# Optimization experiments

Hardware: AMD Instinct MI355X
Metric: run time of the kernel (lower is better)

Reference implementation:

```python
import jax, jax.numpy as jnp
import numpy as np

N, E = 50000, 800000
IN, HID, OUT, EH = 128, 64, 128, 32  # node dims, edge-MLP hidden=32
N_ETYPES, N_NTYPES = 3, 2


def setup_inputs() -> dict:
    key = jax.random.key(0)
    ks = jax.random.split(key, 12)
    w = lambda k, shape, fan: jax.random.normal(k, shape, jnp.float32) / np.float32(np.sqrt(fan))
    nf = jax.random.normal(ks[0], (N, IN), jnp.float32)
    edge_index = jax.random.randint(ks[1], (2, E), 0, N, dtype=jnp.int32)
    edge_type = jax.random.randint(ks[2], (E,), 0, N_ETYPES, dtype=jnp.int32)
    node_type = jax.random.randint(ks[3], (N,), 0, N_NTYPES, dtype=jnp.int32)
    return {
        "nf": nf,
        "edge_index": edge_index,
        "edge_type": edge_type,
        "node_type": node_type,
        # layer 0: 128 -> 64
        "eW0": w(ks[4], (N_ETYPES, 2 * IN, EH), 2 * IN),
        "eb0": jax.random.normal(ks[5], (N_ETYPES, EH), jnp.float32) * 0.01,
        "nW0": w(ks[6], (N_NTYPES, N_ETYPES * EH, HID), N_ETYPES * EH),
        "nb0": jax.random.normal(ks[7], (N_NTYPES, HID), jnp.float32) * 0.01,
        # layer 1: 64 -> 128
        "eW1": w(ks[8], (N_ETYPES, 2 * HID, EH), 2 * HID),
        "eb1": jax.random.normal(ks[9], (N_ETYPES, EH), jnp.float32) * 0.01,
        "nW1": w(ks[10], (N_NTYPES, N_ETYPES * EH, OUT), N_ETYPES * EH),
        "nb1": jax.random.normal(ks[11], (N_NTYPES, OUT), jnp.float32) * 0.01,
    }


def _layer(nf, eW, eb, nW, nb, src, dst, edge_type, node_type):
    """One GraphNeuralNetLayer: per-edge-type message MLP + mean-scatter, then per-node-type update MLP."""
    n = nf.shape[0]
    # edge gather + concat: [E, 2*in]
    feat = jnp.concatenate([nf[src], nf[dst]], axis=-1)
    msgs = []
    for e in range(eW.shape[0]):  # fixed, small number of edge types
        m = jax.nn.relu(feat @ eW[e] + eb[e])            # [E, EH]
        mask = (edge_type == e).astype(nf.dtype)          # select this edge type
        s = jax.ops.segment_sum(m * mask[:, None], dst, num_segments=n)
        cnt = jax.ops.segment_sum(mask, dst, num_segments=n)
        # mean over mailbox; nodes with no type-e in-edges get zeros
        msgs.append(s / jnp.maximum(cnt, 1.0)[:, None])
    h = jnp.concatenate(msgs, axis=-1)                    # [N, 3*EH]
    out0 = jax.nn.relu(h @ nW[0] + nb[0])
    out1 = jax.nn.relu(h @ nW[1] + nb[1])
    return jnp.where((node_type == 0)[:, None], out0, out1)


def reference(nf, edge_index, edge_type, node_type, eW0, eb0, nW0, nb0, eW1, eb1, nW1, nb1):
    src, dst = edge_index[0], edge_index[1]
    h = _layer(nf, eW0, eb0, nW0, nb0, src, dst, edge_type, node_type)   # [N, 64]
    return _layer(h, eW1, eb1, nW1, nb1, src, dst, edge_type, node_type) # [N, 128]
```

## Files before the change

kernel.cpp:

```cpp
#include <hip/hip_runtime.h>


typedef __attribute__((ext_vector_type(8))) short bf16x8_t;
typedef __attribute__((ext_vector_type(4))) float f32x4_t;

__device__ __forceinline__ void cvt_split(float x, unsigned short& h, unsigned short& l) {
  unsigned u = __float_as_uint(x);
  unsigned rh = u + 0x7FFFu + ((u >> 16) & 1u);
  h = (unsigned short)(rh >> 16);
  float xh = __uint_as_float((unsigned)h << 16);
  float xl = x - xh;
  unsigned v = __float_as_uint(xl);
  unsigned rl = v + 0x7FFFu + ((v >> 16) & 1u);
  l = (unsigned short)(rl >> 16);
}


__global__ __launch_bounds__(256) void rank_kernel(const int* __restrict__ dst,
                                                   int* __restrict__ deg8,
                                                   int* __restrict__ rank, int E) {
  int i = blockIdx.x * 256 + threadIdx.x;
  if (i < E) {
    int d = dst[i];
    int r = (i >> 8) & 7;
    rank[i] = atomicAdd(&deg8[d * 8 + r], 1);
  }
}

__global__ __launch_bounds__(256) void scan1_kernel(int* __restrict__ deg8,
                                                    int* __restrict__ rowstart,
                                                    int* __restrict__ bsum, int n) {
  __shared__ int tmp[256];
  int t = threadIdx.x;
  int base = blockIdx.x * 1024 + t * 4;
  int vdeg[4];
#pragma unroll
  for (int q = 0; q < 4; ++q) {
    int v = base + q;
    int d = 0;
    if (v < n) {
      int4 a = *(int4*)(deg8 + (size_t)v * 8);
      int4 b = *(int4*)(deg8 + (size_t)v * 8 + 4);
      int p1 = a.x, p2 = p1 + a.y, p3 = p2 + a.z, p4 = p3 + a.w;
      int p5 = p4 + b.x, p6 = p5 + b.y, p7 = p6 + b.z;
      d = p7 + b.w;
      *(int4*)(deg8 + (size_t)v * 8) = make_int4(0, p1, p2, p3);
      *(int4*)(deg8 + (size_t)v * 8 + 4) = make_int4(p4, p5, p6, p7);
    }
    vdeg[q] = d;
  }
  int s = vdeg[0] + vdeg[1] + vdeg[2] + vdeg[3];
  tmp[t] = s;
  __syncthreads();
  for (int off = 1; off < 256; off <<= 1) {
    int u = (t >= off) ? tmp[t - off] : 0;
    __syncthreads();
    tmp[t] += u;
    __syncthreads();
  }
  int excl = tmp[t] - s;
  if (base < n)     rowstart[base]     = excl;
  if (base + 1 < n) rowstart[base + 1] = excl + vdeg[0];
  if (base + 2 < n) rowstart[base + 2] = excl + vdeg[0] + vdeg[1];
  if (base + 3 < n) rowstart[base + 3] = excl + vdeg[0] + vdeg[1] + vdeg[2];
  if (t == 255) bsum[blockIdx.x] = tmp[255];
}

__global__ __launch_bounds__(64) void scan2_kernel(const int* __restrict__ bsum,
                                                   int* __restrict__ boff, int nb,
                                                   int* __restrict__ rowstart, int n) {
  int lane = threadIdx.x;
  int v = (lane < nb) ? bsum[lane] : 0;
  int incl = v;
  for (int off = 1; off < 64; off <<= 1) {
    int u = __shfl_up(incl, off, 64);
    if (lane >= off) incl += u;
  }
  if (lane < nb) boff[lane] = incl - v;
  if (lane == 63) rowstart[n] = incl;
}

__global__ __launch_bounds__(256) void scan3_kernel(int* __restrict__ rowstart,
                                                    const int* __restrict__ boff, int n) {
  int i = blockIdx.x * 256 + threadIdx.x;
  if (i < n) rowstart[i] += boff[i >> 10];
}

__global__ __launch_bounds__(256) void fill_kernel(const int* __restrict__ src,
                                                   const int* __restrict__ dst,
                                                   const int* __restrict__ etype,
                                                   const int* __restrict__ rank,
                                                   const int* __restrict__ rowstart,
                                                   const int* __restrict__ deg8,
                                                   int* __restrict__ edata, int E) {
  int i = blockIdx.x * 256 + threadIdx.x;
  if (i < E) {
    int d = dst[i];
    int r = (i >> 8) & 7;
    int et = etype[i];
    int pos = rowstart[d] + deg8[d * 8 + r] + rank[i];
    edata[pos] = src[i] * 768 + et * 129;
  }
}


__global__ __launch_bounds__(256) void partition_kernel(const int* __restrict__ ntype,
                                                        int* __restrict__ idxbuf,
                                                        int* __restrict__ tcnt,
                                                        int n, int ncap) {
  int i = blockIdx.x * 256 + threadIdx.x;
  int lane = threadIdx.x & 63;
  int t = (i < n) ? ntype[i] : -1;
  unsigned long long m0 = __ballot(t == 0);
  unsigned long long m1 = __ballot(t == 1);
  int b0 = 0, b1 = 0;
  if (lane == 0) {
    b0 = atomicAdd(&tcnt[0], (int)__popcll(m0));
    b1 = atomicAdd(&tcnt[1], (int)__popcll(m1));
  }
  b0 = __shfl(b0, 0);
  b1 = __shfl(b1, 0);
  unsigned long long below = (1ull << lane) - 1ull;
  if (t == 0) idxbuf[b0 + (int)__popcll(m0 & below)] = i;
  else if (t == 1) idxbuf[ncap + b1 + (int)__popcll(m1 & below)] = i;
}


template <int IN>
__global__ __launch_bounds__(256) void prep_w(const float* __restrict__ eW,
                                              float* __restrict__ wfh,
                                              float* __restrict__ wfl) {
  constexpr int KC = IN / 32;
  int id = blockIdx.x * 256 + threadIdx.x;
  if (id >= 12 * KC * 64) return;
  int lane = id & 63;
  int fk = id >> 6;
  int kc = fk % KC, ct = fk / KC;
  int n = ct * 16 + (lane & 15);
  int kb = kc * 32 + ((lane >> 4) & 3) * 8;
  int half = (n >= 96) ? 1 : 0;
  int jj = n - 96 * half;
  int e = jj >> 5, o = jj & 31;
  const float* wp = eW + ((size_t)((e * 2 + half) * IN) + kb) * 32 + o;
  bf16x8_t hv, lv;
#pragma unroll
  for (int j = 0; j < 8; ++j) {
    unsigned short h, l;
    cvt_split(wp[(size_t)j * 32], h, l);
    hv[j] = (short)h;
    lv[j] = (short)l;
  }
  *(bf16x8_t*)(wfh + (size_t)id * 4) = hv;
  *(bf16x8_t*)(wfl + (size_t)id * 4) = lv;
}


template <int IN>
__global__ __launch_bounds__(256) void proj_mfma(const float* __restrict__ X,
                                                 const float* __restrict__ wfh,
                                                 const float* __restrict__ wfl,
                                                 float* __restrict__ P, int n) {
  constexpr int KC = IN / 32;
  __shared__ short Ah[4 * KC * 64 * 8];
  __shared__ short Al[4 * KC * 64 * 8];
  const int tx = threadIdx.x;
  const int base = blockIdx.x * 64;

  for (int q = tx; q < 4 * KC * 64; q += 256) {
    int lane = q & 63;
    int fk = q >> 6;
    int kc = fk % KC, nt = fk / KC;
    int node = base + nt * 16 + (lane & 15);
    int kb = kc * 32 + ((lane >> 4) & 3) * 8;
    float xs[8];
    if (node < n) {
      float4 a = *(const float4*)(X + (size_t)node * IN + kb);
      float4 b = *(const float4*)(X + (size_t)node * IN + kb + 4);
      xs[0] = a.x; xs[1] = a.y; xs[2] = a.z; xs[3] = a.w;
      xs[4] = b.x; xs[5] = b.y; xs[6] = b.z; xs[7] = b.w;
    } else {
#pragma unroll
      for (int j = 0; j < 8; ++j) xs[j] = 0.f;
    }
    bf16x8_t hv, lv;
#pragma unroll
    for (int j = 0; j < 8; ++j) {
      unsigned short h, l;
      cvt_split(xs[j], h, l);
      hv[j] = (short)h;
      lv[j] = (short)l;
    }
    *(bf16x8_t*)(Ah + (size_t)q * 8) = hv;
    *(bf16x8_t*)(Al + (size_t)q * 8) = lv;
  }
  __syncthreads();

  const int wave = tx >> 6;
  const int lane = tx & 63;

  f32x4_t acc[4][3];
#pragma unroll
  for (int nt = 0; nt < 4; ++nt)
#pragma unroll
    for (int c = 0; c < 3; ++c) acc[nt][c] = (f32x4_t){0.f, 0.f, 0.f, 0.f};

  for (int kc = 0; kc < KC; ++kc) {
    bf16x8_t Bh[3], Bl[3];
#pragma unroll
    for (int c = 0; c < 3; ++c) {
      int ct = wave * 3 + c;
      size_t idx = ((size_t)(ct * KC + kc) * 64 + lane) * 4;
      Bh[c] = *(const bf16x8_t*)(wfh + idx);
      Bl[c] = *(const bf16x8_t*)(wfl + idx);
    }
#pragma unroll
    for (int nt = 0; nt < 4; ++nt) {
      size_t idx = ((size_t)(nt * KC + kc) * 64 + lane) * 8;
      bf16x8_t ah = *(const bf16x8_t*)(Ah + idx);
      bf16x8_t al = *(const bf16x8_t*)(Al + idx);
#pragma unroll
      for (int c = 0; c < 3; ++c) {
        acc[nt][c] = __builtin_amdgcn_mfma_f32_16x16x32_bf16(ah, Bh[c], acc[nt][c], 0, 0, 0);
        acc[nt][c] = __builtin_amdgcn_mfma_f32_16x16x32_bf16(ah, Bl[c], acc[nt][c], 0, 0, 0);
        acc[nt][c] = __builtin_amdgcn_mfma_f32_16x16x32_bf16(al, Bh[c], acc[nt][c], 0, 0, 0);
      }
    }
  }

  const int row0 = ((lane >> 4) & 3) * 4;
  const int col = lane & 15;
#pragma unroll
  for (int nt = 0; nt < 4; ++nt) {
#pragma unroll
    for (int c = 0; c < 3; ++c) {
      int jcol = (wave * 3 + c) * 16 + col;
#pragma unroll
      for (int r = 0; r < 4; ++r) {
        int node = base + nt * 16 + row0 + r;
        if (node < n) P[(size_t)node * 192 + jcol] = acc[nt][c][r];
      }
    }
  }
}


#define ACC_EDGE(pk, v)                                      \
  {                                                          \
    int et_ = (pk) & 3;                                      \
    float pb_ = (et_ == 0) ? pdb0 : ((et_ == 1) ? pdb1 : pdb2); \
    float m_ = fmaxf((v) + pb_, 0.f);                        \
    a0 += (et_ == 0) ? m_ : 0.f;                             \
    a1 += (et_ == 1) ? m_ : 0.f;                             \
    a2 += (et_ == 2) ? m_ : 0.f;                             \
    c0 += (et_ == 0);                                        \
    c1 += (et_ == 1);                                        \
  }

__global__ __launch_bounds__(256) void aggregate_kernel(const float* __restrict__ P,
                                                        const int* __restrict__ rowstart,
                                                        const int* __restrict__ edata,
                                                        const float* __restrict__ eb,
                                                        float* __restrict__ h, int n) {
  int wid = (blockIdx.x * 256 + threadIdx.x) >> 6;
  if (wid >= n) return;
  int lane = threadIdx.x & 63;
  int o = lane & 31, slot = lane >> 5;
  const float* Pd = P + (size_t)wid * 192 + 96;
  float pdb0 = Pd[o] + eb[o];
  float pdb1 = Pd[32 + o] + eb[32 + o];
  float pdb2 = Pd[64 + o] + eb[64 + o];
  int s = rowstart[wid], e = rowstart[wid + 1];
  const char* Pb = (const char*)P;
  int o4 = o * 4;
  float a0 = 0.f, a1 = 0.f, a2 = 0.f;
  int c0 = 0, c1 = 0;
  int i = s + slot;
  for (; i + 6 < e; i += 8) {
    int p0 = edata[i];
    int p1 = edata[i + 2];
    int p2 = edata[i + 4];
    int p3 = edata[i + 6];
    float v0 = *(const float*)(Pb + (p0 & ~3) + o4);
    float v1 = *(const float*)(Pb + (p1 & ~3) + o4);
    float v2 = *(const float*)(Pb + (p2 & ~3) + o4);
    float v3 = *(const float*)(Pb + (p3 & ~3) + o4);
    ACC_EDGE(p0, v0)
    ACC_EDGE(p1, v1)
    ACC_EDGE(p2, v2)
    ACC_EDGE(p3, v3)
  }
  for (; i < e; i += 2) {
    int pk = edata[i];
    float v = *(const float*)(Pb + (pk & ~3) + o4);
    ACC_EDGE(pk, v)
  }
  a0 += __shfl_xor(a0, 32);
  a1 += __shfl_xor(a1, 32);
  a2 += __shfl_xor(a2, 32);
  c0 += __shfl_xor(c0, 32);
  c1 += __shfl_xor(c1, 32);
  if (slot == 0) {
    int total = e - s;
    float* hn = h + (size_t)wid * 96;
    hn[o] = a0 / fmaxf((float)c0, 1.f);
    hn[32 + o] = a1 / fmaxf((float)c1, 1.f);
    hn[64 + o] = a2 / fmaxf((float)(total - c0 - c1), 1.f);
  }
}


template <int OUT>
__global__ __launch_bounds__(256) void mlp2_kernel(const float* __restrict__ H,
                                                   const float* __restrict__ nW,
                                                   const float* __restrict__ nb,
                                                   const int* __restrict__ idxbuf,
                                                   const int* __restrict__ tcnt,
                                                   float* __restrict__ out, int ncap) {
  constexpr int CO = OUT / 32;
  __shared__ float Xs[64 * 32];
  __shared__ float Ws[8 * OUT * 4];

  int c0 = tcnt[0];
  int nb0 = (c0 + 63) >> 6;
  int t, base, cnt;
  if ((int)blockIdx.x < nb0) {
    t = 0; base = blockIdx.x << 6; cnt = c0;
  } else {
    t = 1; base = ((int)blockIdx.x - nb0) << 6; cnt = tcnt[1];
    if (base >= cnt) return;
  }
  const float* W = nW + (size_t)t * 96 * OUT;
  const float* bias = nb + t * OUT;
  const int* il = idxbuf + (size_t)t * ncap;

  const int tx = threadIdx.x;
  const int t32 = tx & 31;
  const int ng = tx >> 5;

  float acc[8][CO];
#pragma unroll
  for (int i = 0; i < 8; ++i)
#pragma unroll
    for (int c = 0; c < CO; ++c) acc[i][c] = 0.f;

  for (int k0 = 0; k0 < 96; k0 += 32) {
    for (int id = tx; id < 512; id += 256) {
      int i = id >> 3, kk4 = (id & 7) * 4;
      float4 v = make_float4(0.f, 0.f, 0.f, 0.f);
      if (base + i < cnt) {
        int row = il[base + i];
        v = *(const float4*)(H + (size_t)row * 96 + k0 + kk4);
      }
      *(float4*)(Xs + i * 32 + kk4) = v;
    }
    for (int id = tx; id < 8 * OUT; id += 256) {
      int g = id / OUT;
      int j = id % OUT;
      const float* wp = W + (size_t)(k0 + 4 * g) * OUT + j;
      float4 v = make_float4(wp[0], wp[OUT], wp[2 * OUT], wp[3 * OUT]);
      *(float4*)(Ws + (size_t)id * 4) = v;
    }
    __syncthreads();
#pragma unroll
    for (int g = 0; g < 8; ++g) {
      float4 xv[8], wv[CO];
#pragma unroll
      for (int i = 0; i < 8; ++i) xv[i] = *(const float4*)(Xs + (ng * 8 + i) * 32 + 4 * g);
#pragma unroll
      for (int c = 0; c < CO; ++c) wv[c] = *(const float4*)(Ws + ((size_t)g * OUT + t32 + 32 * c) * 4);
#pragma unroll
      for (int i = 0; i < 8; ++i)
#pragma unroll
        for (int c = 0; c < CO; ++c) {
          acc[i][c] = fmaf(xv[i].x, wv[c].x, acc[i][c]);
          acc[i][c] = fmaf(xv[i].y, wv[c].y, acc[i][c]);
          acc[i][c] = fmaf(xv[i].z, wv[c].z, acc[i][c]);
          acc[i][c] = fmaf(xv[i].w, wv[c].w, acc[i][c]);
        }
    }
    __syncthreads();
  }

  float bj[CO];
#pragma unroll
  for (int c = 0; c < CO; ++c) bj[c] = bias[t32 + 32 * c];
#pragma unroll
  for (int i = 0; i < 8; ++i) {
    int slot = base + ng * 8 + i;
    if (slot < cnt) {
      int row = il[slot];
#pragma unroll
      for (int c = 0; c < CO; ++c)
        out[(size_t)row * OUT + t32 + 32 * c] = fmaxf(acc[i][c] + bj[c], 0.f);
    }
  }
}


extern "C" void kernel_launch(void* const* d_in, const int* in_sizes, int n_in,
                              void* d_out, int out_size, void* d_ws, size_t ws_size,
                              hipStream_t stream) {
  const float* nf    = (const float*)d_in[0];
  const int*   eidx  = (const int*)d_in[1];
  const int*   etype = (const int*)d_in[2];
  const int*   ntype = (const int*)d_in[3];
  const float* eW0   = (const float*)d_in[4];
  const float* eb0   = (const float*)d_in[5];
  const float* nW0   = (const float*)d_in[6];
  const float* nb0   = (const float*)d_in[7];
  const float* eW1   = (const float*)d_in[8];
  const float* eb1   = (const float*)d_in[9];
  const float* nW1   = (const float*)d_in[10];
  const float* nb1   = (const float*)d_in[11];
  const int N = in_sizes[3];
  const int E = in_sizes[2];
  const int* srcv = eidx;
  const int* dstv = eidx + E;

  float* P   = (float*)d_ws;
  float* h96 = P + (size_t)N * 192;
  float* h64 = h96 + (size_t)N * 96;
  int* rowstart = (int*)(h64 + (size_t)N * 64);
  int* tcnt     = rowstart + ((N + 4) & ~3);
  int* bsum     = tcnt + 2;
  int* boff     = bsum + 64;
  int* idxbuf   = boff + 64;
  int* edata    = idxbuf + 2 * N;
  float* wf0h   = (float*)(edata + E);
  float* wf0l   = wf0h + 12288;
  float* wf1h   = wf0l + 12288;
  float* wf1l   = wf1h + 6144;
  int* rank     = (int*)h96;
  int* deg8     = (int*)h64;

  const int nsb = (N + 1023) / 1024;
  const int egrid = (E + 255) / 256;

  hipMemsetAsync(deg8, 0, (size_t)N * 8 * sizeof(int), stream);
  hipMemsetAsync(tcnt, 0, 2 * sizeof(int), stream);
  prep_w<128><<<12, 256, 0, stream>>>(eW0, wf0h, wf0l);
  prep_w<64><<<6, 256, 0, stream>>>(eW1, wf1h, wf1l);
  rank_kernel<<<egrid, 256, 0, stream>>>(dstv, deg8, rank, E);
  scan1_kernel<<<nsb, 256, 0, stream>>>(deg8, rowstart, bsum, N);
  scan2_kernel<<<1, 64, 0, stream>>>(bsum, boff, nsb, rowstart, N);
  scan3_kernel<<<(N + 255) / 256, 256, 0, stream>>>(rowstart, boff, N);
  fill_kernel<<<egrid, 256, 0, stream>>>(srcv, dstv, etype, rank, rowstart, deg8, edata, E);
  partition_kernel<<<(N + 255) / 256, 256, 0, stream>>>(ntype, idxbuf, tcnt, N, N);

  const int pgrid = (N + 63) / 64;
  int agrid = (N + 3) / 4;
  int mgrid = (N + 63) / 64 + 2;

  proj_mfma<128><<<pgrid, 256, 0, stream>>>(nf, wf0h, wf0l, P, N);
  aggregate_kernel<<<agrid, 256, 0, stream>>>(P, rowstart, edata, eb0, h96, N);
  mlp2_kernel<64><<<mgrid, 256, 0, stream>>>(h96, nW0, nb0, idxbuf, tcnt, h64, N);

  proj_mfma<64><<<pgrid, 256, 0, stream>>>(h64, wf1h, wf1l, P, N);
  aggregate_kernel<<<agrid, 256, 0, stream>>>(P, rowstart, edata, eb1, h96, N);
  mlp2_kernel<128><<<mgrid, 256, 0, stream>>>(h96, nW1, nb1, idxbuf, tcnt, (float*)d_out, N);
}
```

Baseline: 319.9 us.

## Merge setup kernels and split aggregate edges into contiguous halves

Fuses the two weight-prep launches into one kernel, folds the tcnt reset into scan2, and merges the node-type partition into scan3, which drops one memset and three launches. The aggregate kernel now gives each half-wave a contiguous half of the edge range, unrolled by 8, instead of interleaved strided edges. This cuts launch overhead and gives more independent loads in flight per lane, at the cost of slightly uneven tails when a node's degree is odd.

```diff
diff --git a/kernel.cpp b/kernel.cpp
--- a/kernel.cpp
+++ b/kernel.cpp
@@ -68,7 +68,8 @@
 
 __global__ __launch_bounds__(64) void scan2_kernel(const int* __restrict__ bsum,
                                                    int* __restrict__ boff, int nb,
-                                                   int* __restrict__ rowstart, int n) {
+                                                   int* __restrict__ rowstart, int n,
+                                                   int* __restrict__ tcnt) {
   int lane = threadIdx.x;
   int v = (lane < nb) ? bsum[lane] : 0;
   int incl = v;
@@ -78,12 +79,31 @@
   }
   if (lane < nb) boff[lane] = incl - v;
   if (lane == 63) rowstart[n] = incl;
-}
-
-__global__ __launch_bounds__(256) void scan3_kernel(int* __restrict__ rowstart,
-                                                    const int* __restrict__ boff, int n) {
+  if (lane < 2) tcnt[lane] = 0;
+}
+
+__global__ __launch_bounds__(256) void scan3_part_kernel(int* __restrict__ rowstart,
+                                                         const int* __restrict__ boff,
+                                                         const int* __restrict__ ntype,
+                                                         int* __restrict__ idxbuf,
+                                                         int* __restrict__ tcnt,
+                                                         int n, int ncap) {
   int i = blockIdx.x * 256 + threadIdx.x;
   if (i < n) rowstart[i] += boff[i >> 10];
+  int lane = threadIdx.x & 63;
+  int t = (i < n) ? ntype[i] : -1;
+  unsigned long long m0 = __ballot(t == 0);
+  unsigned long long m1 = __ballot(t == 1);
+  int b0 = 0, b1 = 0;
+  if (lane == 0) {
+    b0 = atomicAdd(&tcnt[0], (int)__popcll(m0));
+    b1 = atomicAdd(&tcnt[1], (int)__popcll(m1));
+  }
+  b0 = __shfl(b0, 0);
+  b1 = __shfl(b1, 0);
+  unsigned long long below = (1ull << lane) - 1ull;
+  if (t == 0) idxbuf[b0 + (int)__popcll(m0 & below)] = i;
+  else if (t == 1) idxbuf[ncap + b1 + (int)__popcll(m1 & below)] = i;
 }
 
 __global__ __launch_bounds__(256) void fill_kernel(const int* __restrict__ src,
@@ -104,37 +124,12 @@
 }
 
 
-__global__ __launch_bounds__(256) void partition_kernel(const int* __restrict__ ntype,
-                                                        int* __restrict__ idxbuf,
-                                                        int* __restrict__ tcnt,
-                                                        int n, int ncap) {
-  int i = blockIdx.x * 256 + threadIdx.x;
-  int lane = threadIdx.x & 63;
-  int t = (i < n) ? ntype[i] : -1;
-  unsigned long long m0 = __ballot(t == 0);
-  unsigned long long m1 = __ballot(t == 1);
-  int b0 = 0, b1 = 0;
-  if (lane == 0) {
-    b0 = atomicAdd(&tcnt[0], (int)__popcll(m0));
-    b1 = atomicAdd(&tcnt[1], (int)__popcll(m1));
-  }
-  b0 = __shfl(b0, 0);
-  b1 = __shfl(b1, 0);
-  unsigned long long below = (1ull << lane) - 1ull;
-  if (t == 0) idxbuf[b0 + (int)__popcll(m0 & below)] = i;
-  else if (t == 1) idxbuf[ncap + b1 + (int)__popcll(m1 & below)] = i;
-}
-
-
-template <int IN>
-__global__ __launch_bounds__(256) void prep_w(const float* __restrict__ eW,
-                                              float* __restrict__ wfh,
-                                              float* __restrict__ wfl) {
-  constexpr int KC = IN / 32;
-  int id = blockIdx.x * 256 + threadIdx.x;
-  if (id >= 12 * KC * 64) return;
+__device__ __forceinline__ void prep_w_body(const float* __restrict__ eW, int IN,
+                                            int id, float* __restrict__ wfh,
+                                            float* __restrict__ wfl) {
   int lane = id & 63;
   int fk = id >> 6;
+  int KC = IN / 32;
   int kc = fk % KC, ct = fk / KC;
   int n = ct * 16 + (lane & 15);
   int kb = kc * 32 + ((lane >> 4) & 3) * 8;
@@ -152,6 +147,22 @@
   }
   *(bf16x8_t*)(wfh + (size_t)id * 4) = hv;
   *(bf16x8_t*)(wfl + (size_t)id * 4) = lv;
+}
+
+__global__ __launch_bounds__(256) void prep_w_all(const float* __restrict__ eW0,
+                                                  const float* __restrict__ eW1,
+                                                  float* __restrict__ wf0h,
+                                                  float* __restrict__ wf0l,
+                                                  float* __restrict__ wf1h,
+                                                  float* __restrict__ wf1l) {
+  int b = blockIdx.x;
+  int tx = threadIdx.x;
+  if (b < 12) {
+    prep_w_body(eW0, 128, b * 256 + tx, wf0h, wf0l);
+  } else {
+    int id = (b - 12) * 256 + tx;
+    if (id < 1536) prep_w_body(eW1, 64, id, wf1h, wf1l);
+  }
 }
 
 
@@ -270,26 +281,26 @@
   float pdb1 = Pd[32 + o] + eb[32 + o];
   float pdb2 = Pd[64 + o] + eb[64 + o];
   int s = rowstart[wid], e = rowstart[wid + 1];
+  int len = e - s;
+  int half1 = (len + 1) >> 1;
+  int beg = slot ? s + half1 : s;
+  int end = slot ? e : s + half1;
   const char* Pb = (const char*)P;
   int o4 = o * 4;
   float a0 = 0.f, a1 = 0.f, a2 = 0.f;
   int c0 = 0, c1 = 0;
-  int i = s + slot;
-  for (; i + 6 < e; i += 8) {
-    int p0 = edata[i];
-    int p1 = edata[i + 2];
-    int p2 = edata[i + 4];
-    int p3 = edata[i + 6];
-    float v0 = *(const float*)(Pb + (p0 & ~3) + o4);
-    float v1 = *(const float*)(Pb + (p1 & ~3) + o4);
-    float v2 = *(const float*)(Pb + (p2 & ~3) + o4);
-    float v3 = *(const float*)(Pb + (p3 & ~3) + o4);
-    ACC_EDGE(p0, v0)
-    ACC_EDGE(p1, v1)
-    ACC_EDGE(p2, v2)
-    ACC_EDGE(p3, v3)
-  }
-  for (; i < e; i += 2) {
+  int i = beg;
+  for (; i + 7 < end; i += 8) {
+    int pk[8];
+#pragma unroll
+    for (int u = 0; u < 8; ++u) pk[u] = edata[i + u];
+    float v[8];
+#pragma unroll
+    for (int u = 0; u < 8; ++u) v[u] = *(const float*)(Pb + (pk[u] & ~3) + o4);
+#pragma unroll
+    for (int u = 0; u < 8; ++u) ACC_EDGE(pk[u], v[u])
+  }
+  for (; i < end; ++i) {
     int pk = edata[i];
     float v = *(const float*)(Pb + (pk & ~3) + o4);
     ACC_EDGE(pk, v)
@@ -300,11 +311,10 @@
   c0 += __shfl_xor(c0, 32);
   c1 += __shfl_xor(c1, 32);
   if (slot == 0) {
-    int total = e - s;
     float* hn = h + (size_t)wid * 96;
     hn[o] = a0 / fmaxf((float)c0, 1.f);
     hn[32 + o] = a1 / fmaxf((float)c1, 1.f);
-    hn[64 + o] = a2 / fmaxf((float)(total - c0 - c1), 1.f);
+    hn[64 + o] = a2 / fmaxf((float)(len - c0 - c1), 1.f);
   }
 }
 
@@ -437,15 +447,12 @@
   const int egrid = (E + 255) / 256;
 
   hipMemsetAsync(deg8, 0, (size_t)N * 8 * sizeof(int), stream);
-  hipMemsetAsync(tcnt, 0, 2 * sizeof(int), stream);
-  prep_w<128><<<12, 256, 0, stream>>>(eW0, wf0h, wf0l);
-  prep_w<64><<<6, 256, 0, stream>>>(eW1, wf1h, wf1l);
+  prep_w_all<<<18, 256, 0, stream>>>(eW0, eW1, wf0h, wf0l, wf1h, wf1l);
   rank_kernel<<<egrid, 256, 0, stream>>>(dstv, deg8, rank, E);
   scan1_kernel<<<nsb, 256, 0, stream>>>(deg8, rowstart, bsum, N);
-  scan2_kernel<<<1, 64, 0, stream>>>(bsum, boff, nsb, rowstart, N);
-  scan3_kernel<<<(N + 255) / 256, 256, 0, stream>>>(rowstart, boff, N);
+  scan2_kernel<<<1, 64, 0, stream>>>(bsum, boff, nsb, rowstart, N, tcnt);
+  scan3_part_kernel<<<(N + 255) / 256, 256, 0, stream>>>(rowstart, boff, ntype, idxbuf, tcnt, N, N);
   fill_kernel<<<egrid, 256, 0, stream>>>(srcv, dstv, etype, rank, rowstart, deg8, edata, E);
-  partition_kernel<<<(N + 255) / 256, 256, 0, stream>>>(ntype, idxbuf, tcnt, N, N);
 
   const int pgrid = (N + 63) / 64;
   int agrid = (N + 3) / 4;
```

Result: slower. 331.0 us (+3.5%).
